# Optimization experiments

Measured on AMD Instinct MI355X. Metric: run time of the kernel, lower is better.

The kernel has to match this reference:

```python
import jax, jax.numpy as jnp
import numpy as np

EPS_RMS = 1e-6
EPS_NORM = 1e-9


def rmsnorm(x):
    return x * jax.lax.rsqrt(jnp.mean(x * x, axis=-1, keepdims=True) + EPS_RMS)


def apply_rotary(x, cos, sin):
    # x: [b, h, s, d]; cos/sin: [1, 1, s, d//2]
    d2 = x.shape[-1] // 2
    x1, x2 = x[..., :d2], x[..., d2:]
    return jnp.concatenate([x1 * cos - x2 * sin, x1 * sin + x2 * cos], axis=-1)


def setup_inputs() -> dict:
    key = jax.random.key(0)
    ks = jax.random.split(key, 16)
    b, l, e, h = 4, 1024, 2048, 16
    d = e // h
    query = jax.random.normal(ks[0], (b, l, e), jnp.float32)
    keyt = jax.random.normal(ks[1], (b, l, e), jnp.float32)
    value = jax.random.normal(ks[2], (b, l, e), jnp.float32)
    attn_mask = jnp.tril(jnp.ones((l, l), bool))[None, None]  # causal bool mask
    cos = jax.random.normal(ks[3], (1, 1, l, d // 2), jnp.float32)
    sin = jax.random.normal(ks[4], (1, 1, l, d // 2), jnp.float32)
    sc = 0.02
    Wq = jax.random.normal(ks[5], (e, e), jnp.float32) * sc
    bq = jnp.zeros((e,), jnp.float32)
    Wk = jax.random.normal(ks[6], (e, e), jnp.float32) * sc
    bk = jnp.zeros((e,), jnp.float32)
    Wv = jax.random.normal(ks[7], (e, e), jnp.float32) * sc
    bv = jnp.zeros((e,), jnp.float32)
    Wo = jax.random.normal(ks[8], (e, e), jnp.float32) * sc
    bo = jnp.zeros((e,), jnp.float32)
    return dict(query=query, key=keyt, value=value, attn_mask=attn_mask,
                cos=cos, sin=sin, Wq=Wq, bq=bq, Wk=Wk, bk=bk,
                Wv=Wv, bv=bv, Wo=Wo, bo=bo)


def reference(query, key, value, attn_mask, cos, sin, Wq, bq, Wk, bk, Wv, bv, Wo, bo):
    b, l, e = query.shape
    s = key.shape[1]
    h = 16
    d = e // h
    q = (query @ Wq.T + bq).reshape(b, l, h, d).transpose(0, 2, 1, 3)
    k = (key @ Wk.T + bk).reshape(b, s, h, d).transpose(0, 2, 1, 3)
    v = (value @ Wv.T + bv).reshape(b, s, h, d).transpose(0, 2, 1, 3)
    q, k = rmsnorm(q), rmsnorm(k)
    # rotary (self-attention, s == l)
    q = apply_rotary(q, cos[:, :, :s], sin[:, :, :s])
    k = apply_rotary(k, cos[:, :, :s], sin[:, :, :s])
    # SDPA with boolean mask
    scores = jnp.einsum('bhld,bhsd->bhls', q, k) / jnp.sqrt(jnp.float32(d))
    scores = jnp.where(attn_mask, scores, jnp.finfo(scores.dtype).min)
    p = jax.nn.softmax(scores, axis=-1)
    o = jnp.einsum('bhls,bhsd->bhld', p, v)  # [b,h,l,d]
    # post-attention v-orthogonalization (o.shape == v.shape here)
    vnorm = jnp.sqrt(jnp.sum(v * v, axis=-1, keepdims=True))
    vn = v / jnp.maximum(vnorm, EPS_NORM)
    o = o - jnp.sum(o * vn, axis=-1, keepdims=True) * vn
    o = o.transpose(0, 2, 1, 3).reshape(b, l, e)
    return o @ Wo.T + bo
```

## Files before the change

kernel.cpp:

```cpp
#include <hip/hip_runtime.h>

typedef short short8 __attribute__((ext_vector_type(8)));
typedef float f32x4 __attribute__((ext_vector_type(4)));

#define MFMA_BF16 __builtin_amdgcn_mfma_f32_16x16x32_bf16

__device__ __forceinline__ unsigned short f2bf(float f) {
  unsigned int u = __float_as_uint(f);
  u += 0x7fffu + ((u >> 16) & 1u);
  return (unsigned short)(u >> 16);
}
__device__ __forceinline__ float bf2f(unsigned short u) {
  return __uint_as_float(((unsigned int)u) << 16);
}

typedef __attribute__((address_space(1))) const unsigned int as1_u32;
typedef __attribute__((address_space(3))) unsigned int as3_u32;
__device__ __forceinline__ void gld16(const void* g, void* l) {
  __builtin_amdgcn_global_load_lds((as1_u32*)(unsigned long long)g,
                                   (as3_u32*)(unsigned int)(unsigned long long)l,
                                   16, 0, 0);
}

#define VMCNT(n) asm volatile("s_waitcnt vmcnt(" #n ")" ::: "memory")
__device__ __forceinline__ void barrier_raw() {
  asm volatile("" ::: "memory");
  __builtin_amdgcn_s_barrier();
  asm volatile("" ::: "memory");
}

struct CvtArgs {
  const float* s[7];
  unsigned short* d[7];
  int n8[7];
};

__global__ __launch_bounds__(256) void cvtall(CvtArgs a) {
  const int seg = blockIdx.y;
  int i = blockIdx.x * 256 + threadIdx.x;
  if (i >= a.n8[seg]) return;
  const float4* s4 = (const float4*)a.s[seg];
  float4 x = s4[2 * i], y = s4[2 * i + 1];
  short8 o = {(short)f2bf(x.x), (short)f2bf(x.y), (short)f2bf(x.z), (short)f2bf(x.w),
              (short)f2bf(y.x), (short)f2bf(y.y), (short)f2bf(y.z), (short)f2bf(y.w)};
  *(short8*)&a.d[seg][(size_t)i * 8] = o;
}

struct GemmArgs {
  const unsigned short* A[3];
  const unsigned short* W[3];
  const float* bias[3];
  unsigned short* Cb[3];
  float* Cf;
};

template <bool OUTBF, int NZ>
__global__ __launch_bounds__(512, 2) void gemm_bf16(GemmArgs g) {
  extern __shared__ unsigned short Sh[];
  const int B = blockIdx.x;
  const int z = B >> 8;
  const int i = B & 255;
  const int xcd = i & 7;
  const int q = i >> 3;
  const int bn = (q >> 1) * 128;
  const int bm = (xcd * 2 + (q & 1)) * 256;
  const int K = 2048, N = 2048, NT = 64;
  const int RS = 12288;

  const unsigned short* __restrict__ A = g.A[z];
  const unsigned short* __restrict__ W = g.W[z];
  const float* __restrict__ bias = g.bias[z];
  unsigned short* __restrict__ Cb = g.Cb[z];

  const int t = threadIdx.x, lane = t & 63, w = t >> 6;
  const int wr = w >> 1, wc = w & 1;
  const int quad = lane >> 4, l16 = lane & 15;

  const int sk = ((lane & 3) * 8) ^ (((lane >> 3) & 3) << 3);
  const int srow = lane >> 2;
  const size_t gA0 = (size_t)(bm + w * 32 + srow) * K + sk;
  const size_t gA1 = (size_t)(bm + w * 32 + 16 + srow) * K + sk;
  const size_t gB  = (size_t)(bn + w * 16 + srow) * K + sk;
  const int lA0 = (w * 32) * 32;
  const int lA1 = (w * 32 + 16) * 32;
  const int lB  = 8192 + (w * 16) * 32;

#define STAGE(tt, ring)                                   \
  do {                                                    \
    const int kq = (tt) * 32;                             \
    unsigned short* Ld = &Sh[(ring) * RS];                \
    gld16(A + gA0 + kq, Ld + lA0);                        \
    gld16(A + gA1 + kq, Ld + lA1);                        \
    gld16(W + gB + kq, Ld + lB);                          \
  } while (0)

  const int ka = (quad * 8) ^ (((l16 >> 1) & 3) << 3);
  const int raA = (wr * 64 + l16) * 32 + ka;
  const int raB = 8192 + (wc * 64 + l16) * 32 + ka;

  const f32x4 fz = {0.f, 0.f, 0.f, 0.f};
  f32x4 acc[4][4];
  for (int a = 0; a < 4; ++a)
    for (int b = 0; b < 4; ++b) acc[a][b] = fz;

  STAGE(0, 0);
  STAGE(1, 1);
  STAGE(2, 2);
  VMCNT(6);
  barrier_raw();

#pragma unroll 4
  for (int tt = 0; tt < NT; ++tt) {
    const unsigned short* Sr = &Sh[(tt & 3) * RS];
    short8 af[4], bv[4];
    for (int mt = 0; mt < 4; ++mt)
      af[mt] = *(const short8*)&Sr[raA + mt * 512];
    for (int nt = 0; nt < 4; ++nt)
      bv[nt] = *(const short8*)&Sr[raB + nt * 512];
    if (tt + 3 < NT) STAGE(tt + 3, (tt + 3) & 3);
    barrier_raw();
    __builtin_amdgcn_s_setprio(1);
    for (int mt = 0; mt < 4; ++mt)
      for (int nt = 0; nt < 4; ++nt)
        acc[mt][nt] = MFMA_BF16(af[mt], bv[nt], acc[mt][nt], 0, 0, 0);
    __builtin_amdgcn_s_setprio(0);
    if (tt < NT - 3) VMCNT(6);
    else if (tt == NT - 3) VMCNT(3);
    else if (tt == NT - 2) VMCNT(0);
    barrier_raw();
  }
#undef STAGE

  for (int mt = 0; mt < 4; ++mt)
    for (int nt = 0; nt < 4; ++nt) {
      int row = bm + wr * 64 + mt * 16 + quad * 4;
      int col = bn + wc * 64 + nt * 16 + l16;
      float bc = bias[col];
      for (int r2 = 0; r2 < 4; ++r2) {
        float v = acc[mt][nt][r2] + bc;
        if (OUTBF) Cb[(size_t)(row + r2) * N + col] = f2bf(v);
        else       g.Cf[(size_t)(row + r2) * N + col] = v;
      }
    }
}

__global__ __launch_bounds__(256) void rmsvt(
    const unsigned short* __restrict__ Qf, const unsigned short* __restrict__ Kf,
    const unsigned short* __restrict__ Vf,
    const float* __restrict__ cosT, const float* __restrict__ sinT,
    unsigned short* __restrict__ Qb, unsigned short* __restrict__ Kb,
    unsigned short* __restrict__ Vt) {
  __shared__ unsigned short Vsh[64 * 136];
  if (blockIdx.x < 16384) {
    const int rid = blockIdx.x * 4 + (threadIdx.x >> 6);
    const int lane = threadIdx.x & 63;
    const int li = rid & 1023;
    const int bh = rid >> 10;
    const int hi = bh & 15, bi = bh >> 4;
    const int src = (bi * 1024 + li) * 2048 + hi * 128;
    const int dst = rid * 128;
    const float c = cosT[li * 64 + lane];
    const float s = sinT[li * 64 + lane];

    float q1 = bf2f(Qf[src + lane]), q2 = bf2f(Qf[src + 64 + lane]);
    float ss = q1 * q1 + q2 * q2;
    for (int off = 32; off; off >>= 1) ss += __shfl_xor(ss, off, 64);
    float r = rsqrtf(ss * (1.f / 128.f) + 1e-6f);
    float qa = q1 * r, qb2 = q2 * r;
    const float qsc = 0.08838834764831845f * 1.4426950408889634f;
    Qb[dst + lane]      = f2bf((qa * c - qb2 * s) * qsc);
    Qb[dst + 64 + lane] = f2bf((qa * s + qb2 * c) * qsc);

    float k1 = bf2f(Kf[src + lane]), k2 = bf2f(Kf[src + 64 + lane]);
    float ks = k1 * k1 + k2 * k2;
    for (int off = 32; off; off >>= 1) ks += __shfl_xor(ks, off, 64);
    float rk = rsqrtf(ks * (1.f / 128.f) + 1e-6f);
    float ka = k1 * rk, kb2 = k2 * rk;
    Kb[dst + lane]      = f2bf(ka * c - kb2 * s);
    Kb[dst + 64 + lane] = f2bf(ka * s + kb2 * c);
  } else {
    const int bid = blockIdx.x - 16384;
    const int t = threadIdx.x;
    const int bh = bid >> 4, l0 = (bid & 15) * 64;
    const int hi = bh & 15, bi = bh >> 4;
    {
      int row = t >> 2, c4 = t & 3;
      const unsigned short* src = &Vf[(size_t)(bi * 1024 + l0 + row) * 2048 + hi * 128];
      for (int i = 0; i < 4; ++i) {
        int chunk = c4 * 4 + i;
        *(int4*)&Vsh[row * 136 + chunk * 8] = *(const int4*)&src[chunk * 8];
      }
    }
    __syncthreads();
    {
      int d = t >> 1, half = t & 1;
      unsigned short* dst = &Vt[(size_t)bh * 131072 + (size_t)d * 1024 + l0 + half * 32];
      for (int g = 0; g < 4; ++g) {
        short8 o;
        for (int j = 0; j < 8; ++j)
          o[j] = (short)Vsh[(half * 32 + g * 8 + j) * 136 + d];
        *(short8*)&dst[g * 8] = o;
      }
    }
  }
}

__global__ __launch_bounds__(512, 4) void attn(
    const unsigned short* __restrict__ Qb, const unsigned short* __restrict__ Kb,
    const unsigned short* __restrict__ Vt, unsigned short* __restrict__ Of0,
    unsigned short* __restrict__ Of1, float* __restrict__ Lb) {
  __shared__ unsigned short Kl[64 * 136];
  __shared__ unsigned short Vl[128 * 72];
  __shared__ unsigned short Pl[8][16 * 72];
  const int t = threadIdx.x, lane = t & 63, w = t >> 6;
  const int quad = lane >> 4, l16 = lane & 15;
  const int B = blockIdx.x;
  const int bh = (B & 7) + 8 * ((B >> 3) & 7);
  const int jj = B >> 6;
  const int pair = jj >> 1, split = jj & 1;
  const unsigned short* Qh = Qb + (size_t)bh * 131072;
  const unsigned short* Kh = Kb + (size_t)bh * 131072;
  const unsigned short* Vh = Vt + (size_t)bh * 131072;
  unsigned short* Oh = (split ? Of1 : Of0) + (size_t)bh * 131072;
  float* Lh = Lb + split * 65536 + bh * 1024;

  const int krow = t >> 4, kcol = (t & 15) * 8;
  const int vdr = t >> 3, vc = (t & 7) * 8;
  const f32x4 fz = {0.f, 0.f, 0.f, 0.f};

  for (int ti = 0; ti < 2; ++ti) {
    const int qt = ti == 0 ? 7 - pair : pair;
    const int q0 = qt * 128;

    short8 aQ[4];
    {
      int qr = q0 + w * 16 + l16;
      for (int kk = 0; kk < 4; ++kk)
        aQ[kk] = *(const short8*)&Qh[(size_t)qr * 128 + kk * 32 + quad * 8];
    }
    f32x4 oacc[8];
    for (int i = 0; i < 8; ++i) oacc[i] = fz;
    float Lr[4] = {0.f, 0.f, 0.f, 0.f};
    const int nST = 2 * qt + 2;

    for (int st = split; st < nST; st += 2) {
      const int s0 = st * 64;
      __syncthreads();
      {
        *(int4*)&Kl[krow * 136 + kcol] =
            *(const int4*)&Kh[(size_t)(s0 + krow) * 128 + kcol];
        *(int4*)&Kl[(krow + 32) * 136 + kcol] =
            *(const int4*)&Kh[(size_t)(s0 + krow + 32) * 128 + kcol];
        *(int4*)&Vl[vdr * 72 + vc] =
            *(const int4*)&Vh[(size_t)vdr * 1024 + s0 + vc];
        *(int4*)&Vl[(vdr + 64) * 72 + vc] =
            *(const int4*)&Vh[(size_t)(vdr + 64) * 1024 + s0 + vc];
      }
      __syncthreads();

      f32x4 sfr[4];
      for (int j = 0; j < 4; ++j) sfr[j] = fz;
      for (int kk = 0; kk < 4; ++kk)
        for (int ni = 0; ni < 4; ++ni) {
          short8 bK = *(const short8*)&Kl[(ni * 16 + l16) * 136 + kk * 32 + quad * 8];
          sfr[ni] = MFMA_BF16(aQ[kk], bK, sfr[ni], 0, 0, 0);
        }

      const bool diag = (s0 + 63 > q0);
      for (int r = 0; r < 4; ++r) {
        int q = q0 + w * 16 + quad * 4 + r;
        float ps = 0.f;
        for (int ni = 0; ni < 4; ++ni) {
          float sv = sfr[ni][r];
          if (diag && (s0 + ni * 16 + l16 > q)) sv = -30000.f;
          float pp = exp2f(sv - 16.5f);
          ps += pp;
          Pl[w][(quad * 4 + r) * 72 + ni * 16 + l16] = f2bf(pp);
        }
        ps += __shfl_xor(ps, 1, 64);
        ps += __shfl_xor(ps, 2, 64);
        ps += __shfl_xor(ps, 4, 64);
        ps += __shfl_xor(ps, 8, 64);
        Lr[r] += ps;
      }

      for (int kk = 0; kk < 2; ++kk) {
        short8 aP = *(const short8*)&Pl[w][l16 * 72 + kk * 32 + quad * 8];
        for (int nt = 0; nt < 8; ++nt) {
          short8 bV = *(const short8*)&Vl[(nt * 16 + l16) * 72 + kk * 32 + quad * 8];
          oacc[nt] = MFMA_BF16(aP, bV, oacc[nt], 0, 0, 0);
        }
      }
    }

    for (int r = 0; r < 4; ++r) {
      int q = q0 + w * 16 + quad * 4 + r;
      size_t base = (size_t)q * 128;
      for (int nt = 0; nt < 8; ++nt)
        Oh[base + nt * 16 + l16] = f2bf(oacc[nt][r]);
      if (l16 == 0) Lh[q] = Lr[r];
    }
  }
}

__global__ __launch_bounds__(256) void vnfix(
    const unsigned short* __restrict__ Of0, const unsigned short* __restrict__ Of1,
    const float* __restrict__ Lb, const unsigned short* __restrict__ Vf,
    unsigned short* __restrict__ Op) {
  const int rid = blockIdx.x * 4 + (threadIdx.x >> 6);
  const int lane = threadIdx.x & 63;
  const int li = rid & 1023;
  const int bh = rid >> 10;
  const int hi = bh & 15, bi = bh >> 4;
  const int src = (bi * 1024 + li) * 2048 + hi * 128;
  float inv = 1.f / (Lb[rid] + Lb[65536 + rid]);
  float o1 = (bf2f(Of0[(size_t)rid * 128 + lane]) + bf2f(Of1[(size_t)rid * 128 + lane])) * inv;
  float o2 = (bf2f(Of0[(size_t)rid * 128 + 64 + lane]) + bf2f(Of1[(size_t)rid * 128 + 64 + lane])) * inv;
  float v1 = bf2f(Vf[src + lane]), v2 = bf2f(Vf[src + 64 + lane]);
  float vv = v1 * v1 + v2 * v2;
  float dd = o1 * v1 + o2 * v2;
  for (int off = 32; off; off >>= 1) {
    vv += __shfl_xor(vv, off, 64);
    dd += __shfl_xor(dd, off, 64);
  }
  float vn = fmaxf(sqrtf(vv), 1e-9f);
  float tc = dd / (vn * vn);
  Op[src + lane]      = f2bf(o1 - tc * v1);
  Op[src + 64 + lane] = f2bf(o2 - tc * v2);
}

extern "C" void kernel_launch(void* const* d_in, const int* in_sizes, int n_in,
                              void* d_out, int out_size, void* d_ws, size_t ws_size,
                              hipStream_t stream) {
  const float* query = (const float*)d_in[0];
  const float* key   = (const float*)d_in[1];
  const float* value = (const float*)d_in[2];
  const float* cosT  = (const float*)d_in[4];
  const float* sinT  = (const float*)d_in[5];
  const float* Wq = (const float*)d_in[6];
  const float* bq = (const float*)d_in[7];
  const float* Wk = (const float*)d_in[8];
  const float* bk = (const float*)d_in[9];
  const float* Wv = (const float*)d_in[10];
  const float* bv = (const float*)d_in[11];
  const float* Wo = (const float*)d_in[12];
  const float* bo = (const float*)d_in[13];
  float* out = (float*)d_out;

  char* ws = (char*)d_ws;
  const size_t MB = 1048576;
  unsigned short* Xq  = (unsigned short*)(ws);
  unsigned short* Xk  = (unsigned short*)(ws + 16 * MB);
  unsigned short* Xv  = (unsigned short*)(ws + 32 * MB);
  unsigned short* Wqb = (unsigned short*)(ws + 48 * MB);
  unsigned short* Wkb = (unsigned short*)(ws + 56 * MB);
  unsigned short* Wvb = (unsigned short*)(ws + 64 * MB);
  unsigned short* Wob = (unsigned short*)(ws + 72 * MB);
  unsigned short* Qf  = (unsigned short*)(ws + 80 * MB);
  unsigned short* Kf  = (unsigned short*)(ws + 96 * MB);
  unsigned short* Vf  = (unsigned short*)(ws + 112 * MB);
  unsigned short* Qbb = Xq;
  unsigned short* Kbb = Xk;
  unsigned short* Vtb = Xv;
  unsigned short* Of0 = Qf;
  unsigned short* Of1 = Kf;
  float*          Lbp = (float*)(ws + 64 * MB);
  unsigned short* Opb = (unsigned short*)(ws + 48 * MB);

  CvtArgs ca;
  ca.s[0] = query; ca.d[0] = Xq;  ca.n8[0] = 1048576;
  ca.s[1] = key;   ca.d[1] = Xk;  ca.n8[1] = 1048576;
  ca.s[2] = value; ca.d[2] = Xv;  ca.n8[2] = 1048576;
  ca.s[3] = Wq;    ca.d[3] = Wqb; ca.n8[3] = 524288;
  ca.s[4] = Wk;    ca.d[4] = Wkb; ca.n8[4] = 524288;
  ca.s[5] = Wv;    ca.d[5] = Wvb; ca.n8[5] = 524288;
  ca.s[6] = Wo;    ca.d[6] = Wob; ca.n8[6] = 524288;
  cvtall<<<dim3(4096, 7), 256, 0, stream>>>(ca);

  GemmArgs gp;
  gp.A[0] = Xq;  gp.A[1] = Xk;  gp.A[2] = Xv;
  gp.W[0] = Wqb; gp.W[1] = Wkb; gp.W[2] = Wvb;
  gp.bias[0] = bq; gp.bias[1] = bk; gp.bias[2] = bv;
  gp.Cb[0] = Qf; gp.Cb[1] = Kf; gp.Cb[2] = Vf;
  gp.Cf = nullptr;
  gemm_bf16<true, 3><<<768, 512, 98304, stream>>>(gp);

  rmsvt<<<17408, 256, 0, stream>>>(Qf, Kf, Vf, cosT, sinT, Qbb, Kbb, Vtb);

  attn<<<512, 512, 0, stream>>>(Qbb, Kbb, Vtb, Of0, Of1, Lbp);

  vnfix<<<16384, 256, 0, stream>>>(Of0, Of1, Lbp, Vf, Opb);

  GemmArgs go;
  go.A[0] = Opb; go.A[1] = nullptr; go.A[2] = nullptr;
  go.W[0] = Wob; go.W[1] = nullptr; go.W[2] = nullptr;
  go.bias[0] = bo; go.bias[1] = nullptr; go.bias[2] = nullptr;
  go.Cb[0] = nullptr; go.Cb[1] = nullptr; go.Cb[2] = nullptr;
  go.Cf = out;
  gemm_bf16<false, 1><<<256, 512, 98304, stream>>>(go);
}
```

Before: 430.1 us.

## Restructure GEMM to 4-wave blocks with per-wave larger tiles and triple-buffered LDS

The bf16 GEMM moves from 8 waves per block to 4. Each wave now computes more M rows (MF=8 for the QKV projection, a 128x128 tile with MF=4 for the output projection). The LDS ring drops from 4 stages to 3, with rotating pointers and one barrier per k-step instead of two. The aim is more MFMA work per LDS fragment load, less synchronisation, and, for the output projection, twice as many blocks to fill the GPU. The cost is more accumulator registers per wave and a shallower prefetch depth.

```diff
diff --git a/kernel.cpp b/kernel.cpp
--- a/kernel.cpp
+++ b/kernel.cpp
@@ -22,7 +22,12 @@
                                    16, 0, 0);
 }
 
-#define VMCNT(n) asm volatile("s_waitcnt vmcnt(" #n ")" ::: "memory")
+template <int N>
+__device__ __forceinline__ void vmwait() {
+  if constexpr (N == 0) asm volatile("s_waitcnt vmcnt(0)" ::: "memory");
+  else if constexpr (N == 4) asm volatile("s_waitcnt vmcnt(4)" ::: "memory");
+  else if constexpr (N == 6) asm volatile("s_waitcnt vmcnt(6)" ::: "memory");
+}
 __device__ __forceinline__ void barrier_raw() {
   asm volatile("" ::: "memory");
   __builtin_amdgcn_s_barrier();
@@ -54,18 +59,29 @@
   float* Cf;
 };
 
-template <bool OUTBF, int NZ>
-__global__ __launch_bounds__(512, 2) void gemm_bf16(GemmArgs g) {
+template <bool OUTBF, int NZ, int MF>
+__global__ __launch_bounds__(256, 2) void gemm_bf16(GemmArgs g) {
   extern __shared__ unsigned short Sh[];
+  constexpr int NA = MF / 2;
+  constexpr int L = NA + 2;
+  constexpr int BOFF = MF * 1024;
+  constexpr int RS = MF * 1024 + 4096;
+  const int K = 2048, N = 2048, NT = 64;
+
   const int B = blockIdx.x;
-  const int z = B >> 8;
-  const int i = B & 255;
-  const int xcd = i & 7;
-  const int q = i >> 3;
-  const int bn = (q >> 1) * 128;
-  const int bm = (xcd * 2 + (q & 1)) * 256;
-  const int K = 2048, N = 2048, NT = 64;
-  const int RS = 12288;
+  int z, bm, bn;
+  if constexpr (MF == 8) {
+    z = B >> 8;
+    const int i = B & 255;
+    const int xcd = i & 7, q = i >> 3;
+    bm = (xcd * 2 + (q & 1)) * 256;
+    bn = (q >> 1) * 128;
+  } else {
+    z = 0;
+    const int xcd = B & 7, q = B >> 3;
+    bm = (xcd * 4 + (q & 3)) * 128;
+    bn = (q >> 2) * 128;
+  }
 
   const unsigned short* __restrict__ A = g.A[z];
   const unsigned short* __restrict__ W = g.W[z];
@@ -78,62 +94,65 @@
 
   const int sk = ((lane & 3) * 8) ^ (((lane >> 3) & 3) << 3);
   const int srow = lane >> 2;
-  const size_t gA0 = (size_t)(bm + w * 32 + srow) * K + sk;
-  const size_t gA1 = (size_t)(bm + w * 32 + 16 + srow) * K + sk;
-  const size_t gB  = (size_t)(bn + w * 16 + srow) * K + sk;
-  const int lA0 = (w * 32) * 32;
-  const int lA1 = (w * 32 + 16) * 32;
-  const int lB  = 8192 + (w * 16) * 32;
-
-#define STAGE(tt, ring)                                   \
-  do {                                                    \
-    const int kq = (tt) * 32;                             \
-    unsigned short* Ld = &Sh[(ring) * RS];                \
-    gld16(A + gA0 + kq, Ld + lA0);                        \
-    gld16(A + gA1 + kq, Ld + lA1);                        \
-    gld16(W + gB + kq, Ld + lB);                          \
-  } while (0)
+  size_t gA[NA], gB[2];
+  int lA[NA], lB[2];
+  for (int j = 0; j < NA; ++j) {
+    gA[j] = (size_t)(bm + w * (MF * 8) + j * 16 + srow) * K + sk;
+    lA[j] = (w * (MF * 8) + j * 16) * 32;
+  }
+  for (int j = 0; j < 2; ++j) {
+    gB[j] = (size_t)(bn + w * 32 + j * 16 + srow) * K + sk;
+    lB[j] = BOFF + (w * 32 + j * 16) * 32;
+  }
+
+  auto STAGE = [&](int kq, unsigned short* Ld) {
+    for (int j = 0; j < NA; ++j) gld16(A + gA[j] + kq, Ld + lA[j]);
+    for (int j = 0; j < 2; ++j)  gld16(W + gB[j] + kq, Ld + lB[j]);
+  };
 
   const int ka = (quad * 8) ^ (((l16 >> 1) & 3) << 3);
-  const int raA = (wr * 64 + l16) * 32 + ka;
-  const int raB = 8192 + (wc * 64 + l16) * 32 + ka;
+  const int raA = (wr * (MF * 16) + l16) * 32 + ka;
+  const int raB = BOFF + (wc * 64 + l16) * 32 + ka;
 
   const f32x4 fz = {0.f, 0.f, 0.f, 0.f};
-  f32x4 acc[4][4];
-  for (int a = 0; a < 4; ++a)
+  f32x4 acc[MF][4];
+  for (int a = 0; a < MF; ++a)
     for (int b = 0; b < 4; ++b) acc[a][b] = fz;
 
-  STAGE(0, 0);
-  STAGE(1, 1);
-  STAGE(2, 2);
-  VMCNT(6);
+  unsigned short* cur = Sh;
+  unsigned short* nxt = Sh + RS;
+  unsigned short* stg = Sh + 2 * RS;
+
+  STAGE(0, cur);
+  STAGE(32, nxt);
+  vmwait<L>();
   barrier_raw();
 
-#pragma unroll 4
   for (int tt = 0; tt < NT; ++tt) {
-    const unsigned short* Sr = &Sh[(tt & 3) * RS];
-    short8 af[4], bv[4];
-    for (int mt = 0; mt < 4; ++mt)
-      af[mt] = *(const short8*)&Sr[raA + mt * 512];
+    short8 af[MF], bv[4];
+#pragma unroll
+    for (int mt = 0; mt < MF; ++mt)
+      af[mt] = *(const short8*)&cur[raA + mt * 512];
+#pragma unroll
     for (int nt = 0; nt < 4; ++nt)
-      bv[nt] = *(const short8*)&Sr[raB + nt * 512];
-    if (tt + 3 < NT) STAGE(tt + 3, (tt + 3) & 3);
-    barrier_raw();
+      bv[nt] = *(const short8*)&cur[raB + nt * 512];
+    if (tt + 2 < NT) STAGE((tt + 2) * 32, stg);
     __builtin_amdgcn_s_setprio(1);
-    for (int mt = 0; mt < 4; ++mt)
+#pragma unroll
+    for (int mt = 0; mt < MF; ++mt)
+#pragma unroll
       for (int nt = 0; nt < 4; ++nt)
         acc[mt][nt] = MFMA_BF16(af[mt], bv[nt], acc[mt][nt], 0, 0, 0);
     __builtin_amdgcn_s_setprio(0);
-    if (tt < NT - 3) VMCNT(6);
-    else if (tt == NT - 3) VMCNT(3);
-    else if (tt == NT - 2) VMCNT(0);
+    if (tt < NT - 2) vmwait<L>();
+    else if (tt == NT - 2) vmwait<0>();
     barrier_raw();
-  }
-#undef STAGE
-
-  for (int mt = 0; mt < 4; ++mt)
+    unsigned short* tmp = cur; cur = nxt; nxt = stg; stg = tmp;
+  }
+
+  for (int mt = 0; mt < MF; ++mt)
     for (int nt = 0; nt < 4; ++nt) {
-      int row = bm + wr * 64 + mt * 16 + quad * 4;
+      int row = bm + wr * (MF * 16) + mt * 16 + quad * 4;
       int col = bn + wc * 64 + nt * 16 + l16;
       float bc = bias[col];
       for (int r2 = 0; r2 < 4; ++r2) {
@@ -383,7 +402,7 @@
   gp.bias[0] = bq; gp.bias[1] = bk; gp.bias[2] = bv;
   gp.Cb[0] = Qf; gp.Cb[1] = Kf; gp.Cb[2] = Vf;
   gp.Cf = nullptr;
-  gemm_bf16<true, 3><<<768, 512, 98304, stream>>>(gp);
+  gemm_bf16<true, 3, 8><<<768, 256, 73728, stream>>>(gp);
 
   rmsvt<<<17408, 256, 0, stream>>>(Qf, Kf, Vf, cosT, sinT, Qbb, Kbb, Vtb);
 
@@ -397,5 +416,5 @@
   go.bias[0] = bo; go.bias[1] = nullptr; go.bias[2] = nullptr;
   go.Cb[0] = nullptr; go.Cb[1] = nullptr; go.Cb[2] = nullptr;
   go.Cf = out;
-  gemm_bf16<false, 1><<<256, 512, 98304, stream>>>(go);
-}
+  gemm_bf16<false, 1, 4><<<512, 256, 49152, stream>>>(go);
+}
```

Measured after the change: 439.2 us. +2.1%, slower.
